# Performance work log

Measured on AMD Instinct MI355X. Metric: run time of the kernel, lower is better.

The kernel has to match this reference:

```python
import jax, jax.numpy as jnp
import numpy as np

N = 2048   # num_nodes
DIN = 8    # num_inputs
DC = 8     # comm_channels
DH = 32    # ch_q == dh == dk == FF
K = 2      # message-passing iterations (args.k)


def setup_inputs() -> dict:
    key = jax.random.key(0)
    ks = jax.random.split(key, 16)
    def w(k_, shape):
        return jax.random.normal(k_, shape, dtype=jnp.float32) * 0.05
    return dict(
        x=jax.random.normal(ks[0], (1, N, DIN), dtype=jnp.float32),
        comms=jnp.zeros((1, N, DC), jnp.float32),  # reset comm state
        adj=(jax.random.uniform(ks[1], (N, N)) < 0.01).astype(jnp.float32),
        dense=jax.random.uniform(ks[2], (N, N), dtype=jnp.float32),
        mask=jnp.ones((N,), jnp.float32),
        W_enc=w(ks[3], (DIN + DC, DH)), b_enc=jnp.zeros((DH,), jnp.float32),
        Wq=w(ks[4], (DH, DH)), bq=jnp.zeros((DH,), jnp.float32),
        Wk=w(ks[5], (DH, DH)), bk=jnp.zeros((DH,), jnp.float32),
        Wv=w(ks[6], (DH, DH)), bv=jnp.zeros((DH,), jnp.float32),
        W1=w(ks[7], (3, DH)), b1=jnp.zeros((DH,), jnp.float32),
        W2=w(ks[8], (DH, DH)), b2=jnp.zeros((DH,), jnp.float32),
        W3=w(ks[9], (DH, 1)), b3=jnp.zeros((1,), jnp.float32),
        W_dec=w(ks[10], (DH, 1)), b_dec=jnp.zeros((1,), jnp.float32),
        W_comm=w(ks[11], (DH, DC)), b_comm=jnp.zeros((DC,), jnp.float32),
        k=K,
    )


def _learned_distance(h, adj, dense, Wq, bq, Wk, bk, Wv, bv, W1, b1, W2, b2, W3, b3):
    # h: (N, DH). Torch builds x[i,j] = h[j], y[i,j] = h[i];
    # out[i,j] = q(h_j) . k(h_i)  ==  (K @ Q^T)[i, j]
    q = h @ Wq + bq        # (N, dk)
    kk = h @ Wk + bk       # (N, dk)
    v = h @ Wv + bv        # (N, dh)
    dots = kk @ q.T        # (N, N)
    feats = jnp.stack([dots, adj, dense], axis=-1)   # (N, N, 3)
    f = jax.nn.relu(feats @ W1 + b1)                 # (N, N, FF)
    f = jax.nn.relu(f @ W2 + b2)                     # (N, N, FF)
    logits = (f @ W3 + b3)[..., 0]                   # (N, N)
    focus = jax.nn.softmax(logits, axis=1)           # softmax over dim 1 (j)
    return focus @ v                                 # feature[i] = sum_j focus[i,j] v[j]


def reference(x, comms, adj, dense, mask, W_enc, b_enc, Wq, bq, Wk, bk, Wv, bv,
              W1, b1, W2, b2, W3, b3, W_dec, b_dec, W_comm, b_comm, k):
    inp = jnp.concatenate([x, comms], axis=-1)[0]    # (N, DIN+DC)
    h = inp @ W_enc + b_enc                          # encoding -> (N, ch_q)
    for _ in range(k):                               # k message-passing steps w/ residual
        h = _learned_distance(h, adj, dense, Wq, bq, Wk, bk, Wv, bv,
                              W1, b1, W2, b2, W3, b3) + h
    # comm_decoding is computed in the torch module (state update); it does not
    # feed the returned value: comms_out = tanh(h @ W_comm + b_comm)
    _ = jnp.tanh(h @ W_comm + b_comm)
    out = (h @ W_dec + b_dec)[:, 0]                  # decoding -> (N,)
    neg = jnp.where(mask == 0, -jnp.inf, 0.0).astype(out.dtype)
    return out + neg                                  # non-rl final_feature_process
```

## Files before the change

kernel.cpp:

```cpp
#include <hip/hip_runtime.h>
#include <hip/hip_bf16.h>
#include <math.h>

#define NN 2048

typedef __bf16 bf16x8 __attribute__((ext_vector_type(8)));
typedef float  f32x4  __attribute__((ext_vector_type(4)));

__global__ void k_encqkv(const float* __restrict__ x, const float* __restrict__ comms,
    const float* __restrict__ Wenc, const float* __restrict__ benc,
    const float* __restrict__ Wq, const float* __restrict__ bq,
    const float* __restrict__ Wk, const float* __restrict__ bk,
    const float* __restrict__ Wv, const float* __restrict__ bv,
    float* __restrict__ h, float* __restrict__ q, float* __restrict__ kk, float* __restrict__ v)
{
  int t = threadIdx.x, b = blockIdx.x;
  int r = t >> 5, c = t & 31;
  int row = b*8 + r;
  float acc = benc[c];
  #pragma unroll
  for (int d=0; d<8; ++d) acc = fmaf(x[row*8+d],     Wenc[d*32+c],     acc);
  #pragma unroll
  for (int d=0; d<8; ++d) acc = fmaf(comms[row*8+d], Wenc[(8+d)*32+c], acc);
  __shared__ float hs[8][32];
  hs[r][c] = acc;
  h[row*32+c] = acc;
  __syncthreads();
  float aq=bq[c], ak=bk[c], av=bv[c];
  #pragma unroll 8
  for (int d=0; d<32; ++d){
    float hv = hs[r][d];
    aq = fmaf(hv, Wq[d*32+c], aq);
    ak = fmaf(hv, Wk[d*32+c], ak);
    av = fmaf(hv, Wv[d*32+c], av);
  }
  q[row*32+c]=aq; kk[row*32+c]=ak; v[row*32+c]=av;
}

__launch_bounds__(256)
__global__ void k_logits(const float* __restrict__ q, const float* __restrict__ kk,
    const float* __restrict__ adj, const float* __restrict__ dense,
    const float* __restrict__ W1, const float* __restrict__ b1,
    const float* __restrict__ W2, const float* __restrict__ b2,
    const float* __restrict__ W3, const float* __restrict__ b3,
    float* __restrict__ logits)
{
  int t = threadIdx.x;
  int wave = t >> 6;
  int l = t & 63;
  int lj = l & 15, g = l >> 4;
  int j0 = blockIdx.x * 64 + wave * 16;
  int i0 = blockIdx.y * 16;
  int c1b = 8*g;

  const f32x4* kp = (const f32x4*)(kk + (i0+lj)*32 + c1b);
  f32x4 k0 = kp[0], k1 = kp[1];
  const f32x4* qp = (const f32x4*)(q + (j0+lj)*32 + c1b);
  f32x4 q0 = qp[0], q1 = qp[1];
  bf16x8 af, bq8;
  #pragma unroll
  for (int e=0;e<4;++e){
    af[e] = (__bf16)k0[e];  af[4+e] = (__bf16)k1[e];
    bq8[e] = (__bf16)q0[e]; bq8[4+e] = (__bf16)q1[e];
  }
  f32x4 dacc = {0.f,0.f,0.f,0.f};
  dacc = __builtin_amdgcn_mfma_f32_16x16x32_bf16(af, bq8, dacc, 0, 0, 0);

  f32x4 w10a = *(const f32x4*)(W1 + c1b);      f32x4 w10b = *(const f32x4*)(W1 + c1b + 4);
  f32x4 w11a = *(const f32x4*)(W1 + 32 + c1b); f32x4 w11b = *(const f32x4*)(W1 + 32 + c1b + 4);
  f32x4 w12a = *(const f32x4*)(W1 + 64 + c1b); f32x4 w12b = *(const f32x4*)(W1 + 64 + c1b + 4);
  f32x4 b1a  = *(const f32x4*)(b1 + c1b);      f32x4 b1b  = *(const f32x4*)(b1 + c1b + 4);
  bf16x8 w2f0, w2f1;
  #pragma unroll
  for (int e=0;e<8;++e){
    w2f0[e] = (__bf16)W2[(c1b+e)*32 + lj];
    w2f1[e] = (__bf16)W2[(c1b+e)*32 + 16 + lj];
  }
  f32x4 b2lo = *(const f32x4*)(b2 + 4*g);
  f32x4 b2hi = *(const f32x4*)(b2 + 16 + 4*g);
  f32x4 w3lo = *(const f32x4*)(W3 + 4*g);
  f32x4 w3hi = *(const f32x4*)(W3 + 16 + 4*g);
  float b3v = b3[0];

  float adjv[16], denv[16];
  #pragma unroll
  for (int m=0;m<16;++m){
    adjv[m] = adj  [(i0+m)*NN + j0 + lj];
    denv[m] = dense[(i0+m)*NN + j0 + lj];
  }

  #pragma unroll
  for (int m=0;m<16;++m){
    float d = __shfl(dacc[m & 3], ((m >> 2) << 4) + lj, 64);
    bf16x8 f1f;
    #pragma unroll
    for (int e=0;e<4;++e){
      float fa = fmaf(d, w10a[e], fmaf(adjv[m], w11a[e], fmaf(denv[m], w12a[e], b1a[e])));
      f1f[e]   = (__bf16)fmaxf(fa, 0.f);
      float fb = fmaf(d, w10b[e], fmaf(adjv[m], w11b[e], fmaf(denv[m], w12b[e], b1b[e])));
      f1f[4+e] = (__bf16)fmaxf(fb, 0.f);
    }
    f32x4 z = {0.f,0.f,0.f,0.f};
    f32x4 a0 = __builtin_amdgcn_mfma_f32_16x16x32_bf16(w2f0, f1f, z, 0,0,0);
    f32x4 a1 = __builtin_amdgcn_mfma_f32_16x16x32_bf16(w2f1, f1f, z, 0,0,0);
    float tl = 0.f;
    #pragma unroll
    for (int r=0;r<4;++r){
      tl = fmaf(fmaxf(a0[r]+b2lo[r], 0.f), w3lo[r], tl);
      tl = fmaf(fmaxf(a1[r]+b2hi[r], 0.f), w3hi[r], tl);
    }
    tl += __shfl_xor(tl, 16, 64);
    tl += __shfl_xor(tl, 32, 64);
    tl += b3v;
    if (g == 0) logits[(i0+m)*NN + j0 + lj] = tl;
  }
}

template<int LAST>
__launch_bounds__(256)
__global__ void k_pv(const float* __restrict__ logits,
    const float* __restrict__ v, const float* __restrict__ h_in,
    float* __restrict__ h_out,
    const float* __restrict__ Wq, const float* __restrict__ bq,
    const float* __restrict__ Wk, const float* __restrict__ bk,
    const float* __restrict__ Wv, const float* __restrict__ bv,
    float* __restrict__ qn, float* __restrict__ kn, float* __restrict__ vn,
    const float* __restrict__ Wdec, const float* __restrict__ bdec,
    const float* __restrict__ mask, float* __restrict__ out)
{
  int t = threadIdx.x;
  int w = t >> 6;
  int l = t & 63;
  int li = l & 15, g = l >> 4;
  int i0 = blockIdx.x * 16;
  int jw = w * 512;
  const float* lrow = logits + (i0+li)*NN + jw + 8*g;

  f32x4 mx4 = {-INFINITY,-INFINITY,-INFINITY,-INFINITY};
  for (int s=0; s<16; ++s){
    f32x4 p0 = *(const f32x4*)(lrow + s*32);
    f32x4 p1 = *(const f32x4*)(lrow + s*32 + 4);
    #pragma unroll
    for (int e=0;e<4;++e){ mx4[e] = fmaxf(mx4[e], p0[e]); mx4[e] = fmaxf(mx4[e], p1[e]); }
  }
  float mxl = fmaxf(fmaxf(mx4[0],mx4[1]), fmaxf(mx4[2],mx4[3]));
  mxl = fmaxf(mxl, __shfl_xor(mxl, 16, 64));
  mxl = fmaxf(mxl, __shfl_xor(mxl, 32, 64));
  __shared__ float Ms[4][16];
  if (l < 16) Ms[w][l] = mxl;
  __syncthreads();
  float Mrow = fmaxf(fmaxf(Ms[0][li],Ms[1][li]), fmaxf(Ms[2][li],Ms[3][li]));

  f32x4 acc0 = {0.f,0.f,0.f,0.f}, acc1 = {0.f,0.f,0.f,0.f};
  float Lp = 0.f;
  for (int s=0; s<16; ++s){
    int jb = jw + s*32 + 8*g;
    f32x4 p0 = *(const f32x4*)(lrow + s*32);
    f32x4 p1 = *(const f32x4*)(lrow + s*32 + 4);
    bf16x8 pf;
    #pragma unroll
    for (int e=0;e<4;++e){
      float e0 = __expf(p0[e] - Mrow);
      __bf16 r0 = (__bf16)e0; pf[e]   = r0; Lp += (float)r0;
      float e1 = __expf(p1[e] - Mrow);
      __bf16 r1 = (__bf16)e1; pf[4+e] = r1; Lp += (float)r1;
    }
    bf16x8 vf0, vf1;
    #pragma unroll
    for (int e=0;e<8;++e){
      vf0[e] = (__bf16)v[(jb+e)*32 + li];
      vf1[e] = (__bf16)v[(jb+e)*32 + 16 + li];
    }
    acc0 = __builtin_amdgcn_mfma_f32_16x16x32_bf16(pf, vf0, acc0, 0,0,0);
    acc1 = __builtin_amdgcn_mfma_f32_16x16x32_bf16(pf, vf1, acc1, 0,0,0);
  }
  Lp += __shfl_xor(Lp, 16, 64);
  Lp += __shfl_xor(Lp, 32, 64);
  __shared__ float accs[4][16][32];
  __shared__ float Ls[4][16];
  __shared__ float hsn[16][32];
  #pragma unroll
  for (int r=0;r<4;++r){
    accs[w][4*g+r][li]    = acc0[r];
    accs[w][4*g+r][16+li] = acc1[r];
  }
  if (l < 16) Ls[w][l] = Lp;
  __syncthreads();
  for (int o = t; o < 512; o += 256){
    int i = o >> 5, c = o & 31;
    float s4 = accs[0][i][c] + accs[1][i][c] + accs[2][i][c] + accs[3][i][c];
    float L4 = Ls[0][i] + Ls[1][i] + Ls[2][i] + Ls[3][i];
    float hnew = h_in[(i0+i)*32 + c] + s4 / L4;
    hsn[i][c] = hnew;
    if (!LAST) h_out[(i0+i)*32+c] = hnew;
  }
  __syncthreads();
  if (!LAST){
    for (int o = t; o < 512; o += 256){
      int i = o >> 5, c = o & 31;
      float aq = bq[c], ak = bk[c], av = bv[c];
      #pragma unroll 8
      for (int d=0; d<32; ++d){
        float hv = hsn[i][d];
        aq = fmaf(hv, Wq[d*32+c], aq);
        ak = fmaf(hv, Wk[d*32+c], ak);
        av = fmaf(hv, Wv[d*32+c], av);
      }
      qn[(i0+i)*32+c] = aq; kn[(i0+i)*32+c] = ak; vn[(i0+i)*32+c] = av;
    }
  } else {
    __shared__ float red[16][16];
    int ii = t >> 4, cs = t & 15;
    float part = hsn[ii][2*cs]*Wdec[2*cs] + hsn[ii][2*cs+1]*Wdec[2*cs+1];
    red[ii][cs] = part;
    __syncthreads();
    if (t < 16){
      float sacc = 0.f;
      #pragma unroll
      for (int e=0;e<16;++e) sacc += red[t][e];
      float o = sacc + bdec[0];
      float mk = mask[i0+t];
      out[i0+t] = o + (mk == 0.f ? -INFINITY : 0.f);
    }
  }
}

extern "C" void kernel_launch(void* const* d_in, const int* in_sizes, int n_in,
                              void* d_out, int out_size, void* d_ws, size_t ws_size,
                              hipStream_t stream)
{
  const float* x     = (const float*)d_in[0];
  const float* comms = (const float*)d_in[1];
  const float* adj   = (const float*)d_in[2];
  const float* dense = (const float*)d_in[3];
  const float* mask  = (const float*)d_in[4];
  const float* Wenc  = (const float*)d_in[5];
  const float* benc  = (const float*)d_in[6];
  const float* Wq    = (const float*)d_in[7];
  const float* bq    = (const float*)d_in[8];
  const float* Wk    = (const float*)d_in[9];
  const float* bk    = (const float*)d_in[10];
  const float* Wv    = (const float*)d_in[11];
  const float* bv    = (const float*)d_in[12];
  const float* W1    = (const float*)d_in[13];
  const float* b1    = (const float*)d_in[14];
  const float* W2    = (const float*)d_in[15];
  const float* b2    = (const float*)d_in[16];
  const float* W3    = (const float*)d_in[17];
  const float* b3    = (const float*)d_in[18];
  const float* Wdec  = (const float*)d_in[19];
  const float* bdec  = (const float*)d_in[20];
  float* out = (float*)d_out;

  float* logits = (float*)d_ws;
  float* h1 = logits + (size_t)NN*NN;
  float* h2 = h1 + NN*32;
  float* q1 = h2 + NN*32;
  float* k1 = q1 + NN*32;
  float* v1 = k1 + NN*32;
  float* q2 = v1 + NN*32;
  float* k2 = q2 + NN*32;
  float* v2 = k2 + NN*32;

  k_encqkv<<<256, 256, 0, stream>>>(x, comms, Wenc, benc, Wq,bq,Wk,bk,Wv,bv,
                                    h1, q1, k1, v1);
  dim3 gl(32, 128);
  k_logits<<<gl, 256, 0, stream>>>(q1, k1, adj, dense, W1,b1,W2,b2,W3,b3, logits);
  k_pv<0><<<128, 256, 0, stream>>>(logits, v1, h1, h2,
                                   Wq,bq,Wk,bk,Wv,bv, q2,k2,v2,
                                   nullptr, nullptr, nullptr, nullptr);
  k_logits<<<gl, 256, 0, stream>>>(q2, k2, adj, dense, W1,b1,W2,b2,W3,b3, logits);
  k_pv<1><<<128, 256, 0, stream>>>(logits, v2, h2, nullptr,
                                   nullptr,nullptr,nullptr,nullptr,nullptr,nullptr,
                                   nullptr,nullptr,nullptr,
                                   Wdec, bdec, mask, out);
}
```

Baseline: 120.3 us.

## Pre-pack V as bf16 fragments and use packed FMA/convert in logits MLP

V is now written directly as bf16 in an MFMA-fragment layout (8 rows interleaved per column), so the PV kernel loads each B operand with one 16-byte load instead of eight strided fp32 loads and conversions. The logits MLP uses inline-asm v_pk_fma_f32 and v_cvt_pk_bf16_f32 to halve the VALU instruction count. It folds the b2 bias into the MFMA accumulator initialiser and replaces per-row dot shuffles with an LDS table. The softmax normaliser now sums fp32 exponentials rather than their bf16-rounded values, which slightly changes numerics.

```diff
diff --git a/kernel.cpp b/kernel.cpp
--- a/kernel.cpp
+++ b/kernel.cpp
@@ -6,13 +6,28 @@
 
 typedef __bf16 bf16x8 __attribute__((ext_vector_type(8)));
 typedef float  f32x4  __attribute__((ext_vector_type(4)));
+typedef float  f32x2  __attribute__((ext_vector_type(2)));
+
+union BF8 { unsigned u[4]; bf16x8 v; };
+
+__device__ __forceinline__ f32x2 pk_fma(f32x2 a, f32x2 b, f32x2 c){
+  f32x2 d;
+  asm("v_pk_fma_f32 %0, %1, %2, %3" : "=v"(d) : "v"(a), "v"(b), "v"(c));
+  return d;
+}
+__device__ __forceinline__ unsigned cvtpk(float lo, float hi){
+  unsigned r;
+  asm("v_cvt_pk_bf16_f32 %0, %1, %2" : "=v"(r) : "v"(lo), "v"(hi));
+  return r;
+}
 
 __global__ void k_encqkv(const float* __restrict__ x, const float* __restrict__ comms,
     const float* __restrict__ Wenc, const float* __restrict__ benc,
     const float* __restrict__ Wq, const float* __restrict__ bq,
     const float* __restrict__ Wk, const float* __restrict__ bk,
     const float* __restrict__ Wv, const float* __restrict__ bv,
-    float* __restrict__ h, float* __restrict__ q, float* __restrict__ kk, float* __restrict__ v)
+    float* __restrict__ h, float* __restrict__ q, float* __restrict__ kk,
+    __bf16* __restrict__ vpk)
 {
   int t = threadIdx.x, b = blockIdx.x;
   int r = t >> 5, c = t & 31;
@@ -34,7 +49,8 @@
     ak = fmaf(hv, Wk[d*32+c], ak);
     av = fmaf(hv, Wv[d*32+c], av);
   }
-  q[row*32+c]=aq; kk[row*32+c]=ak; v[row*32+c]=av;
+  q[row*32+c]=aq; kk[row*32+c]=ak;
+  vpk[b*256 + c*8 + r] = (__bf16)av;
 }
 
 __launch_bounds__(256)
@@ -65,11 +81,18 @@
   }
   f32x4 dacc = {0.f,0.f,0.f,0.f};
   dacc = __builtin_amdgcn_mfma_f32_16x16x32_bf16(af, bq8, dacc, 0, 0, 0);
-
-  f32x4 w10a = *(const f32x4*)(W1 + c1b);      f32x4 w10b = *(const f32x4*)(W1 + c1b + 4);
-  f32x4 w11a = *(const f32x4*)(W1 + 32 + c1b); f32x4 w11b = *(const f32x4*)(W1 + 32 + c1b + 4);
-  f32x4 w12a = *(const f32x4*)(W1 + 64 + c1b); f32x4 w12b = *(const f32x4*)(W1 + 64 + c1b + 4);
-  f32x4 b1a  = *(const f32x4*)(b1 + c1b);      f32x4 b1b  = *(const f32x4*)(b1 + c1b + 4);
+  __shared__ float sdots[4][16][16];
+  #pragma unroll
+  for (int r=0;r<4;++r) sdots[wave][4*g+r][lj] = dacc[r];
+
+  f32x2 w10s[4], w11s[4], w12s[4], b1s[4];
+  #pragma unroll
+  for (int p=0;p<4;++p){
+    w10s[p] = ((const f32x2*)(W1 + c1b))[p];
+    w11s[p] = ((const f32x2*)(W1 + 32 + c1b))[p];
+    w12s[p] = ((const f32x2*)(W1 + 64 + c1b))[p];
+    b1s[p]  = ((const f32x2*)(b1 + c1b))[p];
+  }
   bf16x8 w2f0, w2f1;
   #pragma unroll
   for (int e=0;e<8;++e){
@@ -78,8 +101,10 @@
   }
   f32x4 b2lo = *(const f32x4*)(b2 + 4*g);
   f32x4 b2hi = *(const f32x4*)(b2 + 16 + 4*g);
-  f32x4 w3lo = *(const f32x4*)(W3 + 4*g);
-  f32x4 w3hi = *(const f32x4*)(W3 + 16 + 4*g);
+  f32x2 w3s0 = *(const f32x2*)(W3 + 4*g);
+  f32x2 w3s1 = *(const f32x2*)(W3 + 4*g + 2);
+  f32x2 w3s2 = *(const f32x2*)(W3 + 16 + 4*g);
+  f32x2 w3s3 = *(const f32x2*)(W3 + 16 + 4*g + 2);
   float b3v = b3[0];
 
   float adjv[16], denv[16];
@@ -91,24 +116,25 @@
 
   #pragma unroll
   for (int m=0;m<16;++m){
-    float d = __shfl(dacc[m & 3], ((m >> 2) << 4) + lj, 64);
-    bf16x8 f1f;
+    float d = sdots[wave][m][lj];
+    f32x2 d2 = {d, d};
+    f32x2 a2 = {adjv[m], adjv[m]};
+    f32x2 e2 = {denv[m], denv[m]};
+    BF8 fr;
     #pragma unroll
-    for (int e=0;e<4;++e){
-      float fa = fmaf(d, w10a[e], fmaf(adjv[m], w11a[e], fmaf(denv[m], w12a[e], b1a[e])));
-      f1f[e]   = (__bf16)fmaxf(fa, 0.f);
-      float fb = fmaf(d, w10b[e], fmaf(adjv[m], w11b[e], fmaf(denv[m], w12b[e], b1b[e])));
-      f1f[4+e] = (__bf16)fmaxf(fb, 0.f);
+    for (int p=0;p<4;++p){
+      f32x2 f_ = pk_fma(d2, w10s[p], pk_fma(a2, w11s[p], pk_fma(e2, w12s[p], b1s[p])));
+      fr.u[p] = cvtpk(fmaxf(f_.x, 0.f), fmaxf(f_.y, 0.f));
     }
-    f32x4 z = {0.f,0.f,0.f,0.f};
-    f32x4 a0 = __builtin_amdgcn_mfma_f32_16x16x32_bf16(w2f0, f1f, z, 0,0,0);
-    f32x4 a1 = __builtin_amdgcn_mfma_f32_16x16x32_bf16(w2f1, f1f, z, 0,0,0);
-    float tl = 0.f;
-    #pragma unroll
-    for (int r=0;r<4;++r){
-      tl = fmaf(fmaxf(a0[r]+b2lo[r], 0.f), w3lo[r], tl);
-      tl = fmaf(fmaxf(a1[r]+b2hi[r], 0.f), w3hi[r], tl);
-    }
+    f32x4 a0 = __builtin_amdgcn_mfma_f32_16x16x32_bf16(w2f0, fr.v, b2lo, 0,0,0);
+    f32x4 a1 = __builtin_amdgcn_mfma_f32_16x16x32_bf16(w2f1, fr.v, b2hi, 0,0,0);
+    f32x2 p0 = {fmaxf(a0[0],0.f), fmaxf(a0[1],0.f)};
+    f32x2 p1 = {fmaxf(a0[2],0.f), fmaxf(a0[3],0.f)};
+    f32x2 p2 = {fmaxf(a1[0],0.f), fmaxf(a1[1],0.f)};
+    f32x2 p3 = {fmaxf(a1[2],0.f), fmaxf(a1[3],0.f)};
+    f32x2 z2 = {0.f, 0.f};
+    f32x2 acc2 = pk_fma(p0, w3s0, pk_fma(p1, w3s1, pk_fma(p2, w3s2, pk_fma(p3, w3s3, z2))));
+    float tl = acc2.x + acc2.y;
     tl += __shfl_xor(tl, 16, 64);
     tl += __shfl_xor(tl, 32, 64);
     tl += b3v;
@@ -119,12 +145,12 @@
 template<int LAST>
 __launch_bounds__(256)
 __global__ void k_pv(const float* __restrict__ logits,
-    const float* __restrict__ v, const float* __restrict__ h_in,
+    const __bf16* __restrict__ vpk, const float* __restrict__ h_in,
     float* __restrict__ h_out,
     const float* __restrict__ Wq, const float* __restrict__ bq,
     const float* __restrict__ Wk, const float* __restrict__ bk,
     const float* __restrict__ Wv, const float* __restrict__ bv,
-    float* __restrict__ qn, float* __restrict__ kn, float* __restrict__ vn,
+    float* __restrict__ qn, float* __restrict__ kn, __bf16* __restrict__ vpkn,
     const float* __restrict__ Wdec, const float* __restrict__ bdec,
     const float* __restrict__ mask, float* __restrict__ out)
 {
@@ -157,22 +183,18 @@
     int jb = jw + s*32 + 8*g;
     f32x4 p0 = *(const f32x4*)(lrow + s*32);
     f32x4 p1 = *(const f32x4*)(lrow + s*32 + 4);
-    bf16x8 pf;
+    float ex[8];
     #pragma unroll
-    for (int e=0;e<4;++e){
-      float e0 = __expf(p0[e] - Mrow);
-      __bf16 r0 = (__bf16)e0; pf[e]   = r0; Lp += (float)r0;
-      float e1 = __expf(p1[e] - Mrow);
-      __bf16 r1 = (__bf16)e1; pf[4+e] = r1; Lp += (float)r1;
-    }
-    bf16x8 vf0, vf1;
+    for (int e=0;e<4;++e){ ex[e] = __expf(p0[e] - Mrow); ex[4+e] = __expf(p1[e] - Mrow); }
+    BF8 pfr;
     #pragma unroll
-    for (int e=0;e<8;++e){
-      vf0[e] = (__bf16)v[(jb+e)*32 + li];
-      vf1[e] = (__bf16)v[(jb+e)*32 + 16 + li];
-    }
-    acc0 = __builtin_amdgcn_mfma_f32_16x16x32_bf16(pf, vf0, acc0, 0,0,0);
-    acc1 = __builtin_amdgcn_mfma_f32_16x16x32_bf16(pf, vf1, acc1, 0,0,0);
+    for (int p=0;p<4;++p) pfr.u[p] = cvtpk(ex[2*p], ex[2*p+1]);
+    Lp += ((ex[0]+ex[1])+(ex[2]+ex[3])) + ((ex[4]+ex[5])+(ex[6]+ex[7]));
+    int base = (jb >> 3) * 256;
+    bf16x8 vf0 = *(const bf16x8*)(vpk + base + li*8);
+    bf16x8 vf1 = *(const bf16x8*)(vpk + base + (16+li)*8);
+    acc0 = __builtin_amdgcn_mfma_f32_16x16x32_bf16(pfr.v, vf0, acc0, 0,0,0);
+    acc1 = __builtin_amdgcn_mfma_f32_16x16x32_bf16(pfr.v, vf1, acc1, 0,0,0);
   }
   Lp += __shfl_xor(Lp, 16, 64);
   Lp += __shfl_xor(Lp, 32, 64);
@@ -206,7 +228,9 @@
         ak = fmaf(hv, Wk[d*32+c], ak);
         av = fmaf(hv, Wv[d*32+c], av);
       }
-      qn[(i0+i)*32+c] = aq; kn[(i0+i)*32+c] = ak; vn[(i0+i)*32+c] = av;
+      int row = i0 + i;
+      qn[row*32+c] = aq; kn[row*32+c] = ak;
+      vpkn[(row>>3)*256 + c*8 + (row&7)] = (__bf16)av;
     }
   } else {
     __shared__ float red[16][16];
@@ -257,20 +281,20 @@
   float* h2 = h1 + NN*32;
   float* q1 = h2 + NN*32;
   float* k1 = q1 + NN*32;
-  float* v1 = k1 + NN*32;
-  float* q2 = v1 + NN*32;
+  float* q2 = k1 + NN*32;
   float* k2 = q2 + NN*32;
-  float* v2 = k2 + NN*32;
+  __bf16* vpk1 = (__bf16*)(k2 + NN*32);
+  __bf16* vpk2 = vpk1 + (size_t)NN*32;
 
   k_encqkv<<<256, 256, 0, stream>>>(x, comms, Wenc, benc, Wq,bq,Wk,bk,Wv,bv,
-                                    h1, q1, k1, v1);
+                                    h1, q1, k1, vpk1);
   dim3 gl(32, 128);
   k_logits<<<gl, 256, 0, stream>>>(q1, k1, adj, dense, W1,b1,W2,b2,W3,b3, logits);
-  k_pv<0><<<128, 256, 0, stream>>>(logits, v1, h1, h2,
-                                   Wq,bq,Wk,bk,Wv,bv, q2,k2,v2,
+  k_pv<0><<<128, 256, 0, stream>>>(logits, vpk1, h1, h2,
+                                   Wq,bq,Wk,bk,Wv,bv, q2,k2,vpk2,
                                    nullptr, nullptr, nullptr, nullptr);
   k_logits<<<gl, 256, 0, stream>>>(q2, k2, adj, dense, W1,b1,W2,b2,W3,b3, logits);
-  k_pv<1><<<128, 256, 0, stream>>>(logits, v2, h2, nullptr,
+  k_pv<1><<<128, 256, 0, stream>>>(logits, vpk2, h2, nullptr,
                                    nullptr,nullptr,nullptr,nullptr,nullptr,nullptr,
                                    nullptr,nullptr,nullptr,
                                    Wdec, bdec, mask, out);
```

Result: slower. 141.4 us (+17.6%).

## Switch pairwise MLP and PV to packed fp16 with pre-packed V and weights

Applied to the files above, without the earlier changes.

Moves the bf16 MFMA path to fp16. Q, K and V are stored as fp16 by the producer kernels, and V goes into a row-packed layout so each PV MFMA operand becomes one vector load. The first pairwise layer now runs as packed half2 FMA/max instead of scalar fp32, b2 is folded into the MFMA accumulator, and W1/b1/W2 are pre-converted (W2 transposed) once in the encoder. This is meant to cut per-element conversion and ALU work in the N×N logits kernel and the gather loads in PV, at the cost of fp16 range and rounding risk in the intermediate features.

```diff
diff --git a/kernel.cpp b/kernel.cpp
--- a/kernel.cpp
+++ b/kernel.cpp
@@ -1,20 +1,48 @@
 #include <hip/hip_runtime.h>
 #include <hip/hip_bf16.h>
+#include <hip/hip_fp16.h>
 #include <math.h>
 
 #define NN 2048
 
-typedef __bf16 bf16x8 __attribute__((ext_vector_type(8)));
-typedef float  f32x4  __attribute__((ext_vector_type(4)));
+typedef _Float16 f16x8 __attribute__((ext_vector_type(8)));
+typedef _Float16 h2    __attribute__((ext_vector_type(2)));
+typedef float    f32x4 __attribute__((ext_vector_type(4)));
+
+union H8 { h2 h[4]; f16x8 v; };
+
+__device__ __forceinline__ h2 pkrtz(float a, float b){
+  return __builtin_bit_cast(h2, __builtin_amdgcn_cvt_pkrtz(a, b));
+}
+__device__ __forceinline__ h2 hfma(h2 a, h2 b, h2 c){
+  return __builtin_elementwise_fma(a, b, c);
+}
+__device__ __forceinline__ h2 hmax0(h2 a){
+  h2 z = {(_Float16)0.f, (_Float16)0.f};
+  return __builtin_elementwise_max(a, z);
+}
 
 __global__ void k_encqkv(const float* __restrict__ x, const float* __restrict__ comms,
     const float* __restrict__ Wenc, const float* __restrict__ benc,
     const float* __restrict__ Wq, const float* __restrict__ bq,
     const float* __restrict__ Wk, const float* __restrict__ bk,
     const float* __restrict__ Wv, const float* __restrict__ bv,
-    float* __restrict__ h, float* __restrict__ q, float* __restrict__ kk, float* __restrict__ v)
+    const float* __restrict__ W1, const float* __restrict__ b1,
+    const float* __restrict__ W2,
+    float* __restrict__ h, _Float16* __restrict__ qh, _Float16* __restrict__ kh,
+    _Float16* __restrict__ vpk,
+    _Float16* __restrict__ W1h, _Float16* __restrict__ b1h, _Float16* __restrict__ W2t)
 {
   int t = threadIdx.x, b = blockIdx.x;
+  if (b == 0){
+    if (t < 96) W1h[t] = (_Float16)W1[t];
+    if (t < 32) b1h[t] = (_Float16)b1[t];
+    #pragma unroll
+    for (int idx = t; idx < 1024; idx += 256){
+      int c2 = idx >> 5, c1 = idx & 31;
+      W2t[idx] = (_Float16)W2[c1*32 + c2];
+    }
+  }
   int r = t >> 5, c = t & 31;
   int row = b*8 + r;
   float acc = benc[c];
@@ -34,15 +62,18 @@
     ak = fmaf(hv, Wk[d*32+c], ak);
     av = fmaf(hv, Wv[d*32+c], av);
   }
-  q[row*32+c]=aq; kk[row*32+c]=ak; v[row*32+c]=av;
+  qh[row*32+c] = (_Float16)aq;
+  kh[row*32+c] = (_Float16)ak;
+  vpk[b*256 + c*8 + r] = (_Float16)av;
 }
 
 __launch_bounds__(256)
-__global__ void k_logits(const float* __restrict__ q, const float* __restrict__ kk,
+__global__ void k_logits(const _Float16* __restrict__ qh, const _Float16* __restrict__ kh,
     const float* __restrict__ adj, const float* __restrict__ dense,
-    const float* __restrict__ W1, const float* __restrict__ b1,
-    const float* __restrict__ W2, const float* __restrict__ b2,
-    const float* __restrict__ W3, const float* __restrict__ b3,
+    const _Float16* __restrict__ W1h, const _Float16* __restrict__ b1h,
+    const _Float16* __restrict__ W2t,
+    const float* __restrict__ b2, const float* __restrict__ W3,
+    const float* __restrict__ b3,
     float* __restrict__ logits)
 {
   int t = threadIdx.x;
@@ -53,62 +84,55 @@
   int i0 = blockIdx.y * 16;
   int c1b = 8*g;
 
-  const f32x4* kp = (const f32x4*)(kk + (i0+lj)*32 + c1b);
-  f32x4 k0 = kp[0], k1 = kp[1];
-  const f32x4* qp = (const f32x4*)(q + (j0+lj)*32 + c1b);
-  f32x4 q0 = qp[0], q1 = qp[1];
-  bf16x8 af, bq8;
-  #pragma unroll
-  for (int e=0;e<4;++e){
-    af[e] = (__bf16)k0[e];  af[4+e] = (__bf16)k1[e];
-    bq8[e] = (__bf16)q0[e]; bq8[4+e] = (__bf16)q1[e];
-  }
+  f16x8 af = *(const f16x8*)(kh + (i0+lj)*32 + c1b);
+  f16x8 bq = *(const f16x8*)(qh + (j0+lj)*32 + c1b);
   f32x4 dacc = {0.f,0.f,0.f,0.f};
-  dacc = __builtin_amdgcn_mfma_f32_16x16x32_bf16(af, bq8, dacc, 0, 0, 0);
-
-  f32x4 w10a = *(const f32x4*)(W1 + c1b);      f32x4 w10b = *(const f32x4*)(W1 + c1b + 4);
-  f32x4 w11a = *(const f32x4*)(W1 + 32 + c1b); f32x4 w11b = *(const f32x4*)(W1 + 32 + c1b + 4);
-  f32x4 w12a = *(const f32x4*)(W1 + 64 + c1b); f32x4 w12b = *(const f32x4*)(W1 + 64 + c1b + 4);
-  f32x4 b1a  = *(const f32x4*)(b1 + c1b);      f32x4 b1b  = *(const f32x4*)(b1 + c1b + 4);
-  bf16x8 w2f0, w2f1;
-  #pragma unroll
-  for (int e=0;e<8;++e){
-    w2f0[e] = (__bf16)W2[(c1b+e)*32 + lj];
-    w2f1[e] = (__bf16)W2[(c1b+e)*32 + 16 + lj];
-  }
+  dacc = __builtin_amdgcn_mfma_f32_16x16x32_f16(af, bq, dacc, 0, 0, 0);
+
+  h2 w10[4], w11[4], w12[4], b1v[4];
+  #pragma unroll
+  for (int p=0;p<4;++p){
+    w10[p] = ((const h2*)(W1h      + c1b))[p];
+    w11[p] = ((const h2*)(W1h + 32 + c1b))[p];
+    w12[p] = ((const h2*)(W1h + 64 + c1b))[p];
+    b1v[p] = ((const h2*)(b1h      + c1b))[p];
+  }
+  f16x8 w2f0 = *(const f16x8*)(W2t + lj*32 + c1b);
+  f16x8 w2f1 = *(const f16x8*)(W2t + (16+lj)*32 + c1b);
   f32x4 b2lo = *(const f32x4*)(b2 + 4*g);
   f32x4 b2hi = *(const f32x4*)(b2 + 16 + 4*g);
   f32x4 w3lo = *(const f32x4*)(W3 + 4*g);
   f32x4 w3hi = *(const f32x4*)(W3 + 16 + 4*g);
   float b3v = b3[0];
 
-  float adjv[16], denv[16];
+  h2 adjh[16], denh[16];
   #pragma unroll
   for (int m=0;m<16;++m){
-    adjv[m] = adj  [(i0+m)*NN + j0 + lj];
-    denv[m] = dense[(i0+m)*NN + j0 + lj];
+    float a_ = adj  [(i0+m)*NN + j0 + lj];
+    float d_ = dense[(i0+m)*NN + j0 + lj];
+    adjh[m] = pkrtz(a_, a_);
+    denh[m] = pkrtz(d_, d_);
   }
 
   #pragma unroll
   for (int m=0;m<16;++m){
     float d = __shfl(dacc[m & 3], ((m >> 2) << 4) + lj, 64);
-    bf16x8 f1f;
-    #pragma unroll
-    for (int e=0;e<4;++e){
-      float fa = fmaf(d, w10a[e], fmaf(adjv[m], w11a[e], fmaf(denv[m], w12a[e], b1a[e])));
-      f1f[e]   = (__bf16)fmaxf(fa, 0.f);
-      float fb = fmaf(d, w10b[e], fmaf(adjv[m], w11b[e], fmaf(denv[m], w12b[e], b1b[e])));
-      f1f[4+e] = (__bf16)fmaxf(fb, 0.f);
-    }
-    f32x4 z = {0.f,0.f,0.f,0.f};
-    f32x4 a0 = __builtin_amdgcn_mfma_f32_16x16x32_bf16(w2f0, f1f, z, 0,0,0);
-    f32x4 a1 = __builtin_amdgcn_mfma_f32_16x16x32_bf16(w2f1, f1f, z, 0,0,0);
-    float tl = 0.f;
-    #pragma unroll
-    for (int r=0;r<4;++r){
-      tl = fmaf(fmaxf(a0[r]+b2lo[r], 0.f), w3lo[r], tl);
-      tl = fmaf(fmaxf(a1[r]+b2hi[r], 0.f), w3hi[r], tl);
-    }
+    h2 dh = pkrtz(d, d);
+    H8 fr;
+    #pragma unroll
+    for (int p=0;p<4;++p)
+      fr.h[p] = hmax0(hfma(dh, w10[p], hfma(adjh[m], w11[p], hfma(denh[m], w12[p], b1v[p]))));
+    f32x4 a0 = __builtin_amdgcn_mfma_f32_16x16x32_f16(w2f0, fr.v, b2lo, 0,0,0);
+    f32x4 a1 = __builtin_amdgcn_mfma_f32_16x16x32_f16(w2f1, fr.v, b2hi, 0,0,0);
+    float s0 = fmaxf(a0[0],0.f)*w3lo[0];
+    float s1 = fmaxf(a0[1],0.f)*w3lo[1];
+    s0 = fmaf(fmaxf(a0[2],0.f), w3lo[2], s0);
+    s1 = fmaf(fmaxf(a0[3],0.f), w3lo[3], s1);
+    s0 = fmaf(fmaxf(a1[0],0.f), w3hi[0], s0);
+    s1 = fmaf(fmaxf(a1[1],0.f), w3hi[1], s1);
+    s0 = fmaf(fmaxf(a1[2],0.f), w3hi[2], s0);
+    s1 = fmaf(fmaxf(a1[3],0.f), w3hi[3], s1);
+    float tl = s0 + s1;
     tl += __shfl_xor(tl, 16, 64);
     tl += __shfl_xor(tl, 32, 64);
     tl += b3v;
@@ -119,12 +143,12 @@
 template<int LAST>
 __launch_bounds__(256)
 __global__ void k_pv(const float* __restrict__ logits,
-    const float* __restrict__ v, const float* __restrict__ h_in,
+    const _Float16* __restrict__ vpk, const float* __restrict__ h_in,
     float* __restrict__ h_out,
     const float* __restrict__ Wq, const float* __restrict__ bq,
     const float* __restrict__ Wk, const float* __restrict__ bk,
     const float* __restrict__ Wv, const float* __restrict__ bv,
-    float* __restrict__ qn, float* __restrict__ kn, float* __restrict__ vn,
+    _Float16* __restrict__ qn, _Float16* __restrict__ kn, _Float16* __restrict__ vpkn,
     const float* __restrict__ Wdec, const float* __restrict__ bdec,
     const float* __restrict__ mask, float* __restrict__ out)
 {
@@ -157,22 +181,18 @@
     int jb = jw + s*32 + 8*g;
     f32x4 p0 = *(const f32x4*)(lrow + s*32);
     f32x4 p1 = *(const f32x4*)(lrow + s*32 + 4);
-    bf16x8 pf;
-    #pragma unroll
-    for (int e=0;e<4;++e){
-      float e0 = __expf(p0[e] - Mrow);
-      __bf16 r0 = (__bf16)e0; pf[e]   = r0; Lp += (float)r0;
-      float e1 = __expf(p1[e] - Mrow);
-      __bf16 r1 = (__bf16)e1; pf[4+e] = r1; Lp += (float)r1;
-    }
-    bf16x8 vf0, vf1;
-    #pragma unroll
-    for (int e=0;e<8;++e){
-      vf0[e] = (__bf16)v[(jb+e)*32 + li];
-      vf1[e] = (__bf16)v[(jb+e)*32 + 16 + li];
-    }
-    acc0 = __builtin_amdgcn_mfma_f32_16x16x32_bf16(pf, vf0, acc0, 0,0,0);
-    acc1 = __builtin_amdgcn_mfma_f32_16x16x32_bf16(pf, vf1, acc1, 0,0,0);
+    float ex[8];
+    #pragma unroll
+    for (int e=0;e<4;++e){ ex[e] = __expf(p0[e] - Mrow); ex[4+e] = __expf(p1[e] - Mrow); }
+    H8 pfr;
+    #pragma unroll
+    for (int p=0;p<4;++p) pfr.h[p] = pkrtz(ex[2*p], ex[2*p+1]);
+    Lp += ((ex[0]+ex[1])+(ex[2]+ex[3])) + ((ex[4]+ex[5])+(ex[6]+ex[7]));
+    int base = (jb >> 3) * 256;
+    f16x8 vf0 = *(const f16x8*)(vpk + base + li*8);
+    f16x8 vf1 = *(const f16x8*)(vpk + base + (16+li)*8);
+    acc0 = __builtin_amdgcn_mfma_f32_16x16x32_f16(pfr.v, vf0, acc0, 0,0,0);
+    acc1 = __builtin_amdgcn_mfma_f32_16x16x32_f16(pfr.v, vf1, acc1, 0,0,0);
   }
   Lp += __shfl_xor(Lp, 16, 64);
   Lp += __shfl_xor(Lp, 32, 64);
@@ -206,7 +226,10 @@
         ak = fmaf(hv, Wk[d*32+c], ak);
         av = fmaf(hv, Wv[d*32+c], av);
       }
-      qn[(i0+i)*32+c] = aq; kn[(i0+i)*32+c] = ak; vn[(i0+i)*32+c] = av;
+      int row = i0 + i;
+      qn[row*32+c] = (_Float16)aq;
+      kn[row*32+c] = (_Float16)ak;
+      vpkn[(row>>3)*256 + c*8 + (row&7)] = (_Float16)av;
     }
   } else {
     __shared__ float red[16][16];
@@ -255,22 +278,28 @@
   float* logits = (float*)d_ws;
   float* h1 = logits + (size_t)NN*NN;
   float* h2 = h1 + NN*32;
-  float* q1 = h2 + NN*32;
-  float* k1 = q1 + NN*32;
-  float* v1 = k1 + NN*32;
-  float* q2 = v1 + NN*32;
-  float* k2 = q2 + NN*32;
-  float* v2 = k2 + NN*32;
+  _Float16* qh1  = (_Float16*)(h2 + NN*32);
+  _Float16* kh1  = qh1 + (size_t)NN*32;
+  _Float16* qh2  = kh1 + (size_t)NN*32;
+  _Float16* kh2  = qh2 + (size_t)NN*32;
+  _Float16* vpk1 = kh2 + (size_t)NN*32;
+  _Float16* vpk2 = vpk1 + (size_t)NN*32;
+  _Float16* W1h  = vpk2 + (size_t)NN*32;
+  _Float16* b1h  = W1h + 96;
+  _Float16* W2t  = b1h + 32;
 
   k_encqkv<<<256, 256, 0, stream>>>(x, comms, Wenc, benc, Wq,bq,Wk,bk,Wv,bv,
-                                    h1, q1, k1, v1);
+                                    W1, b1, W2,
+                                    h1, qh1, kh1, vpk1, W1h, b1h, W2t);
   dim3 gl(32, 128);
-  k_logits<<<gl, 256, 0, stream>>>(q1, k1, adj, dense, W1,b1,W2,b2,W3,b3, logits);
-  k_pv<0><<<128, 256, 0, stream>>>(logits, v1, h1, h2,
-                                   Wq,bq,Wk,bk,Wv,bv, q2,k2,v2,
+  k_logits<<<gl, 256, 0, stream>>>(qh1, kh1, adj, dense, W1h, b1h, W2t,
+                                   b2, W3, b3, logits);
+  k_pv<0><<<128, 256, 0, stream>>>(logits, vpk1, h1, h2,
+                                   Wq,bq,Wk,bk,Wv,bv, qh2,kh2,vpk2,
                                    nullptr, nullptr, nullptr, nullptr);
-  k_logits<<<gl, 256, 0, stream>>>(q2, k2, adj, dense, W1,b1,W2,b2,W3,b3, logits);
-  k_pv<1><<<128, 256, 0, stream>>>(logits, v2, h2, nullptr,
+  k_logits<<<gl, 256, 0, stream>>>(qh2, kh2, adj, dense, W1h, b1h, W2t,
+                                   b2, W3, b3, logits);
+  k_pv<1><<<128, 256, 0, stream>>>(logits, vpk2, h2, nullptr,
                                    nullptr,nullptr,nullptr,nullptr,nullptr,nullptr,
                                    nullptr,nullptr,nullptr,
                                    Wdec, bdec, mask, out);
```

New measurement: 96.51 us. 19.8% less time.
